# Optimization experiments

Hardware: AMD Instinct MI355X
Metric: run time of the kernel (lower is better)

## Reference

```python
import jax, jax.numpy as jnp
import numpy as np

N_NODES = 100000
N_EDGES = 1600000
IN_DIM, HID, OUT = 128, 128, 64


def setup_inputs() -> dict:
    key = jax.random.key(0)
    ks = jax.random.split(key, 8)
    x = jax.random.normal(ks[0], (N_NODES, IN_DIM), dtype=jnp.float32)
    edge_index = jax.random.randint(ks[1], (2, N_EDGES), 0, N_NODES, dtype=jnp.int64)
    # Glorot-ish init for GCNConv linear weights (stored as [in, out]).
    W1 = jax.random.normal(ks[2], (IN_DIM, HID), dtype=jnp.float32) * (1.0 / np.sqrt(IN_DIM))
    b1 = jnp.zeros((HID,), dtype=jnp.float32)
    W2 = jax.random.normal(ks[3], (HID, HID), dtype=jnp.float32) * (1.0 / np.sqrt(HID))
    b2 = jnp.zeros((HID,), dtype=jnp.float32)
    W3 = jax.random.normal(ks[4], (HID, OUT), dtype=jnp.float32) * (1.0 / np.sqrt(HID))
    b3 = jnp.zeros((OUT,), dtype=jnp.float32)
    return {"x": x, "W1": W1, "b1": b1, "W2": W2, "b2": b2,
            "W3": W3, "b3": b3, "edge_index": edge_index}


def _gcn_norm(edge_index, num_nodes):
    # GCNConv default: add self loops, symmetric normalization D^{-1/2} A D^{-1/2}.
    loops = jnp.arange(num_nodes, dtype=edge_index.dtype)
    src = jnp.concatenate([edge_index[0], loops])
    dst = jnp.concatenate([edge_index[1], loops])
    deg = jax.ops.segment_sum(jnp.ones_like(dst, dtype=jnp.float32), dst,
                              num_segments=num_nodes)
    dinv = jnp.where(deg > 0, jax.lax.rsqrt(deg), 0.0)
    norm = dinv[src] * dinv[dst]  # [E + N]
    return src, dst, norm


def _gcn_conv(h, W, b, src, dst, norm, num_nodes):
    h = h @ W                                   # transform first (PyG GCNConv)
    msg = h[src] * norm[:, None]                # gather + scale
    agg = jax.ops.segment_sum(msg, dst, num_segments=num_nodes)  # scatter-add
    return agg + b


def _dropout(h, key, p=0.5):
    keep = jax.random.bernoulli(key, 1.0 - p, h.shape)
    return jnp.where(keep, h / (1.0 - p), 0.0)


def reference(x, W1, b1, W2, b2, W3, b3, edge_index):
    num_nodes = x.shape[0]
    src, dst, norm = _gcn_norm(edge_index, num_nodes)
    kd1, kd2 = jax.random.split(jax.random.key(42))
    h = jax.nn.relu(_gcn_conv(x, W1, b1, src, dst, norm, num_nodes))
    h = _dropout(h, kd1)
    h = jax.nn.relu(_gcn_conv(h, W2, b2, src, dst, norm, num_nodes))
    h = _dropout(h, kd2)
    return _gcn_conv(h, W3, b3, src, dst, norm, num_nodes)
```

## Files before the change

kernel.cpp:

```cpp
#include <hip/hip_runtime.h>
#include <stdint.h>

#define NN 100000
#define NE 1600000
#define NMASKW 400000
#define GB_E 6250
#define GB_MASK 1563

typedef float f4 __attribute__((ext_vector_type(4)));
typedef float f2 __attribute__((ext_vector_type(2)));
typedef unsigned short us4 __attribute__((ext_vector_type(4)));
typedef short s16x8 __attribute__((ext_vector_type(8)));

__device__ inline float bf2f(unsigned short u) {
  return __uint_as_float(((uint32_t)u) << 16);
}
__device__ inline unsigned short f2bf(float f) {
  uint32_t u = __float_as_uint(f);
  return (unsigned short)((u + 0x7fffu + ((u >> 16) & 1u)) >> 16);
}
__device__ inline float lo16(uint32_t q) { return __uint_as_float(q << 16); }
__device__ inline float hi16(uint32_t q) { return __uint_as_float(q & 0xffff0000u); }

__host__ __device__ inline void threefry2x32(uint32_t k0, uint32_t k1,
                                             uint32_t x0, uint32_t x1,
                                             uint32_t* y0, uint32_t* y1) {
  uint32_t ks[3] = {k0, k1, k0 ^ k1 ^ 0x1BD11BDAu};
  x0 += ks[0]; x1 += ks[1];
  const uint32_t R[2][4] = {{13u, 15u, 26u, 6u}, {17u, 29u, 16u, 24u}};
#pragma unroll
  for (int i = 0; i < 5; ++i) {
#pragma unroll
    for (int j = 0; j < 4; ++j) {
      uint32_t r = R[i & 1][j];
      x0 += x1;
      x1 = (x1 << r) | (x1 >> (32u - r));
      x1 ^= x0;
    }
    x0 += ks[(i + 1) % 3];
    x1 += ks[(i + 2) % 3] + (uint32_t)(i + 1);
  }
  *y0 = x0; *y1 = x1;
}

__device__ inline uint32_t tf_bits32(uint32_t k0, uint32_t k1, uint32_t idx) {
  uint32_t a, b;
  threefry2x32(k0, k1, 0u, idx, &a, &b);
  return a ^ b;
}

__global__ __launch_bounds__(256) void k_histmask(
    const int* __restrict__ ei, uint32_t* __restrict__ cnt,
    int* __restrict__ slot, uint32_t* __restrict__ m1, uint32_t* __restrict__ m2,
    uint32_t k10, uint32_t k11, uint32_t k20, uint32_t k21) {
  int b = blockIdx.x;
  int q = b / 5, r = b % 5;
  if (r < 4) {
    int e = (q * 4 + r) * 256 + threadIdx.x;
    if (e < NE) {
      int d = ei[NE + e];
      slot[e] = (int)atomicAdd(&cnt[d], 1u);
    }
  } else {
    int t = q * 256 + threadIdx.x;
    if (t < NMASKW) {
      uint32_t base = (uint32_t)t * 32u;
      uint32_t w1 = 0, w2 = 0;
#pragma unroll 4
      for (int j = 0; j < 32; ++j) {
        w1 |= (tf_bits32(k10, k11, base + j) >> 31) << j;
        w2 |= (tf_bits32(k20, k21, base + j) >> 31) << j;
      }
      m1[t] = w1;
      m2[t] = w2;
    }
  }
}

__global__ __launch_bounds__(256) void k_scan1(const uint32_t* __restrict__ cnt,
                                               uint32_t* __restrict__ rp,
                                               uint32_t* __restrict__ bsum,
                                               float* __restrict__ dinv) {
  __shared__ uint32_t sh[256];
  int t = threadIdx.x;
  int base = blockIdx.x * 1024 + t * 4;
  uint32_t v[4];
  uint32_t s = 0;
#pragma unroll
  for (int i = 0; i < 4; ++i) {
    int idx = base + i;
    v[i] = (idx < NN) ? cnt[idx] : 0u;
    if (idx < NN) dinv[idx] = 1.0f / sqrtf((float)(v[i] + 1u));
    s += v[i];
  }
  sh[t] = s;
  __syncthreads();
  for (int off = 1; off < 256; off <<= 1) {
    uint32_t x = sh[t];
    if (t >= off) x += sh[t - off];
    __syncthreads();
    sh[t] = x;
    __syncthreads();
  }
  uint32_t run = (t > 0) ? sh[t - 1] : 0u;
  if (t == 255) bsum[blockIdx.x] = sh[255];
#pragma unroll
  for (int i = 0; i < 4; ++i) {
    int idx = base + i;
    if (idx < NN) rp[idx] = run;
    run += v[i];
  }
}

__global__ void k_scan2(uint32_t* bsum, int nb) {
  if (threadIdx.x == 0 && blockIdx.x == 0) {
    uint32_t s = 0;
    for (int i = 0; i < nb; ++i) { uint32_t x = bsum[i]; bsum[i] = s; s += x; }
  }
}

__global__ void k_scan3(uint32_t* rp, const uint32_t* __restrict__ bsum) {
  int i = blockIdx.x * 256 + threadIdx.x;
  if (i < NN) rp[i] += bsum[i >> 10];
  if (i == 0) rp[NN] = (uint32_t)NE;
}

__global__ void k_scatter(const int* __restrict__ ei,
                          const uint32_t* __restrict__ rp,
                          const int* __restrict__ slot,
                          const float* __restrict__ dinv,
                          uint2* __restrict__ e2) {
  int e = blockIdx.x * 256 + threadIdx.x;
  if (e < NE) {
    int s = ei[e];
    int d = ei[NE + e];
    float w = dinv[s] * dinv[d];
    uint32_t pos = rp[d] + (uint32_t)slot[e];
    uint2 rec;
    rec.x = (uint32_t)s;
    rec.y = __float_as_uint(w);
    e2[pos] = rec;
  }
}

__global__ void k_wsplit3(const float* __restrict__ W1, const float* __restrict__ W2,
                          const float* __restrict__ W3,
                          unsigned short* __restrict__ w1h, unsigned short* __restrict__ w1l,
                          unsigned short* __restrict__ w2h, unsigned short* __restrict__ w2l,
                          unsigned short* __restrict__ w3h, unsigned short* __restrict__ w3l) {
  int b = blockIdx.x;
  const float* W; unsigned short *H, *L; int dout, bb;
  if (b < 32)      { W = W1; H = w1h; L = w1l; dout = 128; bb = b; }
  else if (b < 64) { W = W2; H = w2h; L = w2l; dout = 128; bb = b - 32; }
  else             { W = W3; H = w3h; L = w3l; dout = 64;  bb = b - 64; }
  int lane = threadIdx.x;
  int kk = bb & 3;
  int ct = bb >> 2;
  int kbase = kk * 32 + (lane >> 4) * 8;
  int col = ct * 16 + (lane & 15);
  us4 h0, h1, l0, l1;
#pragma unroll
  for (int j = 0; j < 4; ++j) {
    float v = W[(size_t)(kbase + j) * dout + col];
    h0[j] = f2bf(v);
    l0[j] = f2bf(v - bf2f(h0[j]));
    float v2 = W[(size_t)(kbase + 4 + j) * dout + col];
    h1[j] = f2bf(v2);
    l1[j] = f2bf(v2 - bf2f(h1[j]));
  }
  size_t o = ((size_t)bb * 64 + lane) * 8;
  *(us4*)(H + o) = h0; *(us4*)(H + o + 4) = h1;
  *(us4*)(L + o) = l0; *(us4*)(L + o + 4) = l1;
}

__global__ __launch_bounds__(256) void k_gemm1(
    const float* __restrict__ A, const unsigned short* __restrict__ Wh,
    const unsigned short* __restrict__ Wl, unsigned short* __restrict__ C) {
  constexpr int NT = 8;
  const int w = threadIdx.x >> 6;
  const int lane = threadIdx.x & 63;
  const int row0 = blockIdx.x * 64 + w * 16;
  int ar = row0 + (lane & 15);
  if (ar >= NN) ar = NN - 1;
  const int aoff = (lane >> 4) * 8;
  s16x8 afh[4], afl[4];
#pragma unroll
  for (int kk = 0; kk < 4; ++kk) {
    f4 v0 = *(const f4*)(A + (size_t)ar * 128 + kk * 32 + aoff);
    f4 v1 = *(const f4*)(A + (size_t)ar * 128 + kk * 32 + aoff + 4);
#pragma unroll
    for (int j = 0; j < 4; ++j) {
      unsigned short h = f2bf(v0[j]);
      afh[kk][j] = (short)h;
      afl[kk][j] = (short)f2bf(v0[j] - bf2f(h));
      unsigned short h2 = f2bf(v1[j]);
      afh[kk][j + 4] = (short)h2;
      afl[kk][j + 4] = (short)f2bf(v1[j] - bf2f(h2));
    }
  }
  f4 acc[NT];
#pragma unroll
  for (int t = 0; t < NT; ++t) acc[t] = (f4){0.f, 0.f, 0.f, 0.f};
#pragma unroll
  for (int ct = 0; ct < NT; ++ct) {
#pragma unroll
    for (int kk = 0; kk < 4; ++kk) {
      size_t bo = ((size_t)(ct * 4 + kk) * 64 + lane) * 8;
      s16x8 bh = *(const s16x8*)(Wh + bo);
      s16x8 bl = *(const s16x8*)(Wl + bo);
      acc[ct] = __builtin_amdgcn_mfma_f32_16x16x32_bf16(afh[kk], bh, acc[ct], 0, 0, 0);
      acc[ct] = __builtin_amdgcn_mfma_f32_16x16x32_bf16(afh[kk], bl, acc[ct], 0, 0, 0);
      acc[ct] = __builtin_amdgcn_mfma_f32_16x16x32_bf16(afl[kk], bh, acc[ct], 0, 0, 0);
    }
  }
  const int rbase = row0 + (lane >> 4) * 4;
  const int cbase = lane & 15;
#pragma unroll
  for (int ct = 0; ct < NT; ++ct) {
#pragma unroll
    for (int r = 0; r < 4; ++r) {
      int gr = rbase + r;
      if (gr < NN) C[(size_t)gr * 128 + ct * 16 + cbase] = f2bf(acc[ct][r]);
    }
  }
}

template <int DOUT>
__global__ __launch_bounds__(256) void k_gemm_mfma(
    const unsigned short* __restrict__ Ah, const unsigned short* __restrict__ Al,
    const unsigned short* __restrict__ Wh, const unsigned short* __restrict__ Wl,
    unsigned short* __restrict__ C) {
  constexpr int NT = DOUT / 16;
  const int w = threadIdx.x >> 6;
  const int lane = threadIdx.x & 63;
  const int row0 = blockIdx.x * 64 + w * 16;
  int ar = row0 + (lane & 15);
  if (ar >= NN) ar = NN - 1;
  const int aoff = (lane >> 4) * 8;
  s16x8 afh[4], afl[4];
#pragma unroll
  for (int kk = 0; kk < 4; ++kk) {
    afh[kk] = *(const s16x8*)(Ah + (size_t)ar * 128 + kk * 32 + aoff);
    afl[kk] = *(const s16x8*)(Al + (size_t)ar * 128 + kk * 32 + aoff);
  }
  f4 acc[NT];
#pragma unroll
  for (int t = 0; t < NT; ++t) acc[t] = (f4){0.f, 0.f, 0.f, 0.f};
#pragma unroll
  for (int ct = 0; ct < NT; ++ct) {
#pragma unroll
    for (int kk = 0; kk < 4; ++kk) {
      size_t bo = ((size_t)(ct * 4 + kk) * 64 + lane) * 8;
      s16x8 bh = *(const s16x8*)(Wh + bo);
      s16x8 bl = *(const s16x8*)(Wl + bo);
      acc[ct] = __builtin_amdgcn_mfma_f32_16x16x32_bf16(afh[kk], bh, acc[ct], 0, 0, 0);
      acc[ct] = __builtin_amdgcn_mfma_f32_16x16x32_bf16(afh[kk], bl, acc[ct], 0, 0, 0);
      acc[ct] = __builtin_amdgcn_mfma_f32_16x16x32_bf16(afl[kk], bh, acc[ct], 0, 0, 0);
    }
  }
  const int rbase = row0 + (lane >> 4) * 4;
  const int cbase = lane & 15;
#pragma unroll
  for (int ct = 0; ct < NT; ++ct) {
#pragma unroll
    for (int r = 0; r < 4; ++r) {
      int gr = rbase + r;
      if (gr < NN) C[(size_t)gr * DOUT + ct * 16 + cbase] = f2bf(acc[ct][r]);
    }
  }
}

__global__ __launch_bounds__(256) void k_agg_mid(
    const unsigned short* __restrict__ hb, const uint32_t* __restrict__ rp,
    const uint2* __restrict__ e2, const float* __restrict__ dinv,
    const float* __restrict__ bias, const uint32_t* __restrict__ mask,
    unsigned short* __restrict__ oh, unsigned short* __restrict__ ol) {
  int wid = __builtin_amdgcn_readfirstlane(blockIdx.x * 4 + (threadIdx.x >> 6));
  if (wid >= NN) return;
  const int lane = threadIdx.x & 63;
  const int q = lane >> 4;
  const int fl = lane & 15;
  const uint32_t beg = rp[wid], end = rp[wid + 1];
  const float dv = dinv[wid];
  const float sn = dv * dv;
  const char* hbase = (const char*)hb;
  float acc[8];
#pragma unroll
  for (int j = 0; j < 8; ++j) acc[j] = 0.f;

  uint32_t u = beg;
  for (; u + 8 <= end; u += 8) {
    uint2 r0 = e2[u + q];
    uint2 r1 = e2[u + 4 + q];
    uint4 g0 = *(const uint4*)(hbase + ((size_t)r0.x << 8) + fl * 16);
    uint4 g1 = *(const uint4*)(hbase + ((size_t)r1.x << 8) + fl * 16);
    float w0 = __uint_as_float(r0.y), w1 = __uint_as_float(r1.y);
    acc[0] = fmaf(w0, lo16(g0.x), acc[0]); acc[1] = fmaf(w0, hi16(g0.x), acc[1]);
    acc[2] = fmaf(w0, lo16(g0.y), acc[2]); acc[3] = fmaf(w0, hi16(g0.y), acc[3]);
    acc[4] = fmaf(w0, lo16(g0.z), acc[4]); acc[5] = fmaf(w0, hi16(g0.z), acc[5]);
    acc[6] = fmaf(w0, lo16(g0.w), acc[6]); acc[7] = fmaf(w0, hi16(g0.w), acc[7]);
    acc[0] = fmaf(w1, lo16(g1.x), acc[0]); acc[1] = fmaf(w1, hi16(g1.x), acc[1]);
    acc[2] = fmaf(w1, lo16(g1.y), acc[2]); acc[3] = fmaf(w1, hi16(g1.y), acc[3]);
    acc[4] = fmaf(w1, lo16(g1.z), acc[4]); acc[5] = fmaf(w1, hi16(g1.z), acc[5]);
    acc[6] = fmaf(w1, lo16(g1.w), acc[6]); acc[7] = fmaf(w1, hi16(g1.w), acc[7]);
  }
  for (; u < end; u += 4) {
    uint32_t idx = u + (uint32_t)q;
    uint32_t cidx = idx < end ? idx : end - 1u;
    uint2 r = e2[cidx];
    float w = (idx < end) ? __uint_as_float(r.y) : 0.f;
    uint4 g = *(const uint4*)(hbase + ((size_t)r.x << 8) + fl * 16);
    acc[0] = fmaf(w, lo16(g.x), acc[0]); acc[1] = fmaf(w, hi16(g.x), acc[1]);
    acc[2] = fmaf(w, lo16(g.y), acc[2]); acc[3] = fmaf(w, hi16(g.y), acc[3]);
    acc[4] = fmaf(w, lo16(g.z), acc[4]); acc[5] = fmaf(w, hi16(g.z), acc[5]);
    acc[6] = fmaf(w, lo16(g.w), acc[6]); acc[7] = fmaf(w, hi16(g.w), acc[7]);
  }
#pragma unroll
  for (int j = 0; j < 8; ++j) acc[j] += __shfl_xor(acc[j], 16);
#pragma unroll
  for (int j = 0; j < 8; ++j) acc[j] += __shfl_xor(acc[j], 32);

  uint4 qs = *(const uint4*)(hbase + ((size_t)(uint32_t)wid << 8) + fl * 16);
  f4 b0 = *(const f4*)(bias + fl * 8);
  f4 b1 = *(const f4*)(bias + fl * 8 + 4);
  acc[0] = fmaf(sn, lo16(qs.x), acc[0]) + b0[0];
  acc[1] = fmaf(sn, hi16(qs.x), acc[1]) + b0[1];
  acc[2] = fmaf(sn, lo16(qs.y), acc[2]) + b0[2];
  acc[3] = fmaf(sn, hi16(qs.y), acc[3]) + b0[3];
  acc[4] = fmaf(sn, lo16(qs.z), acc[4]) + b1[0];
  acc[5] = fmaf(sn, hi16(qs.z), acc[5]) + b1[1];
  acc[6] = fmaf(sn, lo16(qs.w), acc[6]) + b1[2];
  acc[7] = fmaf(sn, hi16(qs.w), acc[7]) + b1[3];
  uint32_t mw = mask[(uint32_t)wid * 4u + (uint32_t)(fl >> 2)];
  uint32_t bb = (uint32_t)((fl & 3) * 8);
#pragma unroll
  for (int j = 0; j < 8; ++j) {
    float a = fmaxf(acc[j], 0.f);
    acc[j] = ((mw >> (bb + j)) & 1u) ? 0.f : a * 2.f;
  }
  uint32_t hw[4], lw[4];
#pragma unroll
  for (int j = 0; j < 4; ++j) {
    unsigned short h0 = f2bf(acc[2 * j]), h1 = f2bf(acc[2 * j + 1]);
    unsigned short g0 = f2bf(acc[2 * j] - bf2f(h0));
    unsigned short g1 = f2bf(acc[2 * j + 1] - bf2f(h1));
    hw[j] = (uint32_t)h0 | ((uint32_t)h1 << 16);
    lw[j] = (uint32_t)g0 | ((uint32_t)g1 << 16);
  }
  if (q == 0) {
    uint4 v = {hw[0], hw[1], hw[2], hw[3]};
    *(uint4*)(oh + (size_t)(uint32_t)wid * 128 + fl * 8) = v;
  } else if (q == 1) {
    uint4 v = {lw[0], lw[1], lw[2], lw[3]};
    *(uint4*)(ol + (size_t)(uint32_t)wid * 128 + fl * 8) = v;
  }
}

__global__ __launch_bounds__(256) void k_agg_final(
    const unsigned short* __restrict__ hb, const uint32_t* __restrict__ rp,
    const uint2* __restrict__ e2, const float* __restrict__ dinv,
    const float* __restrict__ bias, float* __restrict__ out) {
  int wid = __builtin_amdgcn_readfirstlane(blockIdx.x * 4 + (threadIdx.x >> 6));
  if (wid >= NN) return;
  const int lane = threadIdx.x & 63;
  const int q = lane >> 4;
  const int fl = lane & 15;
  const uint32_t beg = rp[wid], end = rp[wid + 1];
  const float dv = dinv[wid];
  const float sn = dv * dv;
  const char* hbase = (const char*)hb;
  float acc[4];
#pragma unroll
  for (int j = 0; j < 4; ++j) acc[j] = 0.f;

  uint32_t u = beg;
  for (; u + 8 <= end; u += 8) {
    uint2 r0 = e2[u + q];
    uint2 r1 = e2[u + 4 + q];
    uint2 g0 = *(const uint2*)(hbase + ((size_t)r0.x << 7) + fl * 8);
    uint2 g1 = *(const uint2*)(hbase + ((size_t)r1.x << 7) + fl * 8);
    float w0 = __uint_as_float(r0.y), w1 = __uint_as_float(r1.y);
    acc[0] = fmaf(w0, lo16(g0.x), acc[0]); acc[1] = fmaf(w0, hi16(g0.x), acc[1]);
    acc[2] = fmaf(w0, lo16(g0.y), acc[2]); acc[3] = fmaf(w0, hi16(g0.y), acc[3]);
    acc[0] = fmaf(w1, lo16(g1.x), acc[0]); acc[1] = fmaf(w1, hi16(g1.x), acc[1]);
    acc[2] = fmaf(w1, lo16(g1.y), acc[2]); acc[3] = fmaf(w1, hi16(g1.y), acc[3]);
  }
  for (; u < end; u += 4) {
    uint32_t idx = u + (uint32_t)q;
    uint32_t cidx = idx < end ? idx : end - 1u;
    uint2 r = e2[cidx];
    float w = (idx < end) ? __uint_as_float(r.y) : 0.f;
    uint2 g = *(const uint2*)(hbase + ((size_t)r.x << 7) + fl * 8);
    acc[0] = fmaf(w, lo16(g.x), acc[0]); acc[1] = fmaf(w, hi16(g.x), acc[1]);
    acc[2] = fmaf(w, lo16(g.y), acc[2]); acc[3] = fmaf(w, hi16(g.y), acc[3]);
  }
#pragma unroll
  for (int j = 0; j < 4; ++j) acc[j] += __shfl_xor(acc[j], 16);
#pragma unroll
  for (int j = 0; j < 4; ++j) acc[j] += __shfl_xor(acc[j], 32);

  uint2 qs = *(const uint2*)(hbase + ((size_t)(uint32_t)wid << 7) + fl * 8);
  f4 bv = *(const f4*)(bias + fl * 4);
  acc[0] = fmaf(sn, lo16(qs.x), acc[0]) + bv[0];
  acc[1] = fmaf(sn, hi16(qs.x), acc[1]) + bv[1];
  acc[2] = fmaf(sn, lo16(qs.y), acc[2]) + bv[2];
  acc[3] = fmaf(sn, hi16(qs.y), acc[3]) + bv[3];
  if (q == 0) {
    f4 v = {acc[0], acc[1], acc[2], acc[3]};
    *(f4*)(out + (size_t)(uint32_t)wid * 64 + fl * 4) = v;
  }
}

extern "C" void kernel_launch(void* const* d_in, const int* in_sizes, int n_in,
                              void* d_out, int out_size, void* d_ws, size_t ws_size,
                              hipStream_t stream) {
  (void)in_sizes; (void)n_in; (void)out_size; (void)ws_size;
  const float* x  = (const float*)d_in[0];
  const float* W1 = (const float*)d_in[1];
  const float* b1 = (const float*)d_in[2];
  const float* W2 = (const float*)d_in[3];
  const float* b2 = (const float*)d_in[4];
  const float* W3 = (const float*)d_in[5];
  const float* b3 = (const float*)d_in[6];
  const int* ei   = (const int*)d_in[7];
  float* out = (float*)d_out;

  char* p = (char*)d_ws;
  auto alloc = [&](size_t bytes) -> void* {
    void* r = (void*)p;
    p += (bytes + 255) & ~(size_t)255;
    return r;
  };
  uint32_t* cnt  = (uint32_t*)alloc((size_t)NN * 4);
  float*    dinv = (float*)alloc((size_t)NN * 4);
  uint32_t* rp   = (uint32_t*)alloc((size_t)(NN + 1) * 4);
  uint32_t* bsum = (uint32_t*)alloc(1024);
  int*      slot = (int*)alloc((size_t)NE * 4);
  uint2*    e2   = (uint2*)alloc((size_t)NE * 8);
  uint32_t* m1   = (uint32_t*)alloc((size_t)NMASKW * 4);
  uint32_t* m2   = (uint32_t*)alloc((size_t)NMASKW * 4);
  unsigned short* ah = (unsigned short*)alloc((size_t)NN * 128 * 2);
  unsigned short* al = (unsigned short*)alloc((size_t)NN * 128 * 2);
  unsigned short* hb = (unsigned short*)alloc((size_t)NN * 128 * 2);
  unsigned short* w1h = (unsigned short*)alloc(32 * 64 * 8 * 2);
  unsigned short* w1l = (unsigned short*)alloc(32 * 64 * 8 * 2);
  unsigned short* w2h = (unsigned short*)alloc(32 * 64 * 8 * 2);
  unsigned short* w2l = (unsigned short*)alloc(32 * 64 * 8 * 2);
  unsigned short* w3h = (unsigned short*)alloc(16 * 64 * 8 * 2);
  unsigned short* w3l = (unsigned short*)alloc(16 * 64 * 8 * 2);

  uint32_t kd1a, kd1b, kd2a, kd2b;
  threefry2x32(0u, 42u, 0u, 0u, &kd1a, &kd1b);
  threefry2x32(0u, 42u, 0u, 1u, &kd2a, &kd2b);

  const int gbN = (NN + 255) / 256;
  const int gbE = (NE + 255) / 256;
  const int gbScan = (NN + 1023) / 1024;
  const int gbGemm = (NN + 63) / 64;
  const int gbAgg = (NN + 3) / 4;

  hipMemsetAsync(cnt, 0, (size_t)NN * 4, stream);
  k_histmask<<<8000, 256, 0, stream>>>(ei, cnt, slot, m1, m2, kd1a, kd1b, kd2a, kd2b);
  k_scan1<<<gbScan, 256, 0, stream>>>(cnt, rp, bsum, dinv);
  k_scan2<<<1, 64, 0, stream>>>(bsum, gbScan);
  k_scan3<<<gbN, 256, 0, stream>>>(rp, bsum);
  k_scatter<<<gbE, 256, 0, stream>>>(ei, rp, slot, dinv, e2);
  k_wsplit3<<<80, 64, 0, stream>>>(W1, W2, W3, w1h, w1l, w2h, w2l, w3h, w3l);

  k_gemm1<<<gbGemm, 256, 0, stream>>>(x, w1h, w1l, hb);
  k_agg_mid<<<gbAgg, 256, 0, stream>>>(hb, rp, e2, dinv, b1, m1, ah, al);
  k_gemm_mfma<128><<<gbGemm, 256, 0, stream>>>(ah, al, w2h, w2l, hb);
  k_agg_mid<<<gbAgg, 256, 0, stream>>>(hb, rp, e2, dinv, b2, m2, ah, al);
  k_gemm_mfma<64><<<gbGemm, 256, 0, stream>>>(ah, al, w3h, w3l, hb);
  k_agg_final<<<gbAgg, 256, 0, stream>>>(hb, rp, e2, dinv, b3, out);
}
```

Before: 398.3 us.

## Store CSR as source indices only, compute edge weights on the fly in aggregation

The CSR edge array now holds only 4-byte source indices instead of 8-byte (src, weight) pairs, and the aggregation kernels recompute each edge weight as dinv[src]*dinv[dst] from a small cached table. The edge scatter and weight split are merged into one launch. The mask-generation blocks are reordered ahead of the histogram blocks. The aggregation loops are unrolled to 16 edges per iteration using packed float2 math. This halves edge-stream traffic in three aggregation passes and trims launches, at the cost of an extra dependent gather into dinv per edge.

```diff
diff --git a/kernel.cpp b/kernel.cpp
--- a/kernel.cpp
+++ b/kernel.cpp
@@ -4,8 +4,9 @@
 #define NN 100000
 #define NE 1600000
 #define NMASKW 400000
-#define GB_E 6250
-#define GB_MASK 1563
+#define MASK_BLKS 1563
+#define HIST_BLKS 6250
+#define WSPL_BLKS 20
 
 typedef float f4 __attribute__((ext_vector_type(4)));
 typedef float f2 __attribute__((ext_vector_type(2)));
@@ -54,15 +55,8 @@
     int* __restrict__ slot, uint32_t* __restrict__ m1, uint32_t* __restrict__ m2,
     uint32_t k10, uint32_t k11, uint32_t k20, uint32_t k21) {
   int b = blockIdx.x;
-  int q = b / 5, r = b % 5;
-  if (r < 4) {
-    int e = (q * 4 + r) * 256 + threadIdx.x;
-    if (e < NE) {
-      int d = ei[NE + e];
-      slot[e] = (int)atomicAdd(&cnt[d], 1u);
-    }
-  } else {
-    int t = q * 256 + threadIdx.x;
+  if (b < MASK_BLKS) {
+    int t = b * 256 + threadIdx.x;
     if (t < NMASKW) {
       uint32_t base = (uint32_t)t * 32u;
       uint32_t w1 = 0, w2 = 0;
@@ -74,6 +68,12 @@
       m1[t] = w1;
       m2[t] = w2;
     }
+  } else {
+    int e = (b - MASK_BLKS) * 256 + threadIdx.x;
+    if (e < NE) {
+      int d = ei[NE + e];
+      slot[e] = (int)atomicAdd(&cnt[d], 1u);
+    }
   }
 }
 
@@ -125,52 +125,47 @@
   if (i == 0) rp[NN] = (uint32_t)NE;
 }
 
-__global__ void k_scatter(const int* __restrict__ ei,
-                          const uint32_t* __restrict__ rp,
-                          const int* __restrict__ slot,
-                          const float* __restrict__ dinv,
-                          uint2* __restrict__ e2) {
-  int e = blockIdx.x * 256 + threadIdx.x;
-  if (e < NE) {
-    int s = ei[e];
-    int d = ei[NE + e];
-    float w = dinv[s] * dinv[d];
-    uint32_t pos = rp[d] + (uint32_t)slot[e];
-    uint2 rec;
-    rec.x = (uint32_t)s;
-    rec.y = __float_as_uint(w);
-    e2[pos] = rec;
-  }
-}
-
-__global__ void k_wsplit3(const float* __restrict__ W1, const float* __restrict__ W2,
-                          const float* __restrict__ W3,
-                          unsigned short* __restrict__ w1h, unsigned short* __restrict__ w1l,
-                          unsigned short* __restrict__ w2h, unsigned short* __restrict__ w2l,
-                          unsigned short* __restrict__ w3h, unsigned short* __restrict__ w3l) {
+__global__ __launch_bounds__(256) void k_scatwsplit(
+    const int* __restrict__ ei, const uint32_t* __restrict__ rp,
+    const int* __restrict__ slot, int* __restrict__ csrc,
+    const float* __restrict__ W1, const float* __restrict__ W2,
+    const float* __restrict__ W3,
+    unsigned short* __restrict__ w1h, unsigned short* __restrict__ w1l,
+    unsigned short* __restrict__ w2h, unsigned short* __restrict__ w2l,
+    unsigned short* __restrict__ w3h, unsigned short* __restrict__ w3l) {
   int b = blockIdx.x;
-  const float* W; unsigned short *H, *L; int dout, bb;
-  if (b < 32)      { W = W1; H = w1h; L = w1l; dout = 128; bb = b; }
-  else if (b < 64) { W = W2; H = w2h; L = w2l; dout = 128; bb = b - 32; }
-  else             { W = W3; H = w3h; L = w3l; dout = 64;  bb = b - 64; }
-  int lane = threadIdx.x;
-  int kk = bb & 3;
-  int ct = bb >> 2;
-  int kbase = kk * 32 + (lane >> 4) * 8;
-  int col = ct * 16 + (lane & 15);
-  us4 h0, h1, l0, l1;
-#pragma unroll
-  for (int j = 0; j < 4; ++j) {
-    float v = W[(size_t)(kbase + j) * dout + col];
-    h0[j] = f2bf(v);
-    l0[j] = f2bf(v - bf2f(h0[j]));
-    float v2 = W[(size_t)(kbase + 4 + j) * dout + col];
-    h1[j] = f2bf(v2);
-    l1[j] = f2bf(v2 - bf2f(h1[j]));
-  }
-  size_t o = ((size_t)bb * 64 + lane) * 8;
-  *(us4*)(H + o) = h0; *(us4*)(H + o + 4) = h1;
-  *(us4*)(L + o) = l0; *(us4*)(L + o + 4) = l1;
+  if (b < WSPL_BLKS) {
+    int bb = b * 4 + (threadIdx.x >> 6);
+    int lane = threadIdx.x & 63;
+    const float* W; unsigned short *H, *L; int dout, j0;
+    if (bb < 32)      { W = W1; H = w1h; L = w1l; dout = 128; j0 = bb; }
+    else if (bb < 64) { W = W2; H = w2h; L = w2l; dout = 128; j0 = bb - 32; }
+    else              { W = W3; H = w3h; L = w3l; dout = 64;  j0 = bb - 64; }
+    int kk = j0 & 3;
+    int ct = j0 >> 2;
+    int kbase = kk * 32 + (lane >> 4) * 8;
+    int col = ct * 16 + (lane & 15);
+    us4 h0, h1, l0, l1;
+#pragma unroll
+    for (int j = 0; j < 4; ++j) {
+      float v = W[(size_t)(kbase + j) * dout + col];
+      h0[j] = f2bf(v);
+      l0[j] = f2bf(v - bf2f(h0[j]));
+      float v2 = W[(size_t)(kbase + 4 + j) * dout + col];
+      h1[j] = f2bf(v2);
+      l1[j] = f2bf(v2 - bf2f(h1[j]));
+    }
+    size_t o = ((size_t)j0 * 64 + lane) * 8;
+    *(us4*)(H + o) = h0; *(us4*)(H + o + 4) = h1;
+    *(us4*)(L + o) = l0; *(us4*)(L + o + 4) = l1;
+  } else {
+    int e = (b - WSPL_BLKS) * 256 + threadIdx.x;
+    if (e < NE) {
+      int s = ei[e];
+      int d = ei[NE + e];
+      csrc[rp[d] + (uint32_t)slot[e]] = s;
+    }
+  }
 }
 
 __global__ __launch_bounds__(256) void k_gemm1(
@@ -272,7 +267,7 @@
 
 __global__ __launch_bounds__(256) void k_agg_mid(
     const unsigned short* __restrict__ hb, const uint32_t* __restrict__ rp,
-    const uint2* __restrict__ e2, const float* __restrict__ dinv,
+    const int* __restrict__ csrc, const float* __restrict__ dinv,
     const float* __restrict__ bias, const uint32_t* __restrict__ mask,
     unsigned short* __restrict__ oh, unsigned short* __restrict__ ol) {
   int wid = __builtin_amdgcn_readfirstlane(blockIdx.x * 4 + (threadIdx.x >> 6));
@@ -284,67 +279,74 @@
   const float dv = dinv[wid];
   const float sn = dv * dv;
   const char* hbase = (const char*)hb;
-  float acc[8];
-#pragma unroll
-  for (int j = 0; j < 8; ++j) acc[j] = 0.f;
+  f2 acc[4];
+#pragma unroll
+  for (int j = 0; j < 4; ++j) acc[j] = (f2){0.f, 0.f};
+
+#define ACC4(g, wv)                                                        \
+  {                                                                        \
+    f2 wv2 = {wv, wv};                                                     \
+    f2 h0 = {lo16(g.x), hi16(g.x)}; acc[0] += wv2 * h0;                    \
+    f2 h1 = {lo16(g.y), hi16(g.y)}; acc[1] += wv2 * h1;                    \
+    f2 h2 = {lo16(g.z), hi16(g.z)}; acc[2] += wv2 * h2;                    \
+    f2 h3 = {lo16(g.w), hi16(g.w)}; acc[3] += wv2 * h3;                    \
+  }
 
   uint32_t u = beg;
-  for (; u + 8 <= end; u += 8) {
-    uint2 r0 = e2[u + q];
-    uint2 r1 = e2[u + 4 + q];
-    uint4 g0 = *(const uint4*)(hbase + ((size_t)r0.x << 8) + fl * 16);
-    uint4 g1 = *(const uint4*)(hbase + ((size_t)r1.x << 8) + fl * 16);
-    float w0 = __uint_as_float(r0.y), w1 = __uint_as_float(r1.y);
-    acc[0] = fmaf(w0, lo16(g0.x), acc[0]); acc[1] = fmaf(w0, hi16(g0.x), acc[1]);
-    acc[2] = fmaf(w0, lo16(g0.y), acc[2]); acc[3] = fmaf(w0, hi16(g0.y), acc[3]);
-    acc[4] = fmaf(w0, lo16(g0.z), acc[4]); acc[5] = fmaf(w0, hi16(g0.z), acc[5]);
-    acc[6] = fmaf(w0, lo16(g0.w), acc[6]); acc[7] = fmaf(w0, hi16(g0.w), acc[7]);
-    acc[0] = fmaf(w1, lo16(g1.x), acc[0]); acc[1] = fmaf(w1, hi16(g1.x), acc[1]);
-    acc[2] = fmaf(w1, lo16(g1.y), acc[2]); acc[3] = fmaf(w1, hi16(g1.y), acc[3]);
-    acc[4] = fmaf(w1, lo16(g1.z), acc[4]); acc[5] = fmaf(w1, hi16(g1.z), acc[5]);
-    acc[6] = fmaf(w1, lo16(g1.w), acc[6]); acc[7] = fmaf(w1, hi16(g1.w), acc[7]);
+  for (; u + 16 <= end; u += 16) {
+    int s0 = csrc[u + q];
+    int s1 = csrc[u + 4 + q];
+    int s2 = csrc[u + 8 + q];
+    int s3 = csrc[u + 12 + q];
+    float w0 = dinv[s0] * dv, w1 = dinv[s1] * dv;
+    float w2 = dinv[s2] * dv, w3 = dinv[s3] * dv;
+    uint4 g0 = *(const uint4*)(hbase + ((size_t)(uint32_t)s0 << 8) + fl * 16);
+    uint4 g1 = *(const uint4*)(hbase + ((size_t)(uint32_t)s1 << 8) + fl * 16);
+    uint4 g2 = *(const uint4*)(hbase + ((size_t)(uint32_t)s2 << 8) + fl * 16);
+    uint4 g3 = *(const uint4*)(hbase + ((size_t)(uint32_t)s3 << 8) + fl * 16);
+    ACC4(g0, w0); ACC4(g1, w1); ACC4(g2, w2); ACC4(g3, w3);
   }
   for (; u < end; u += 4) {
     uint32_t idx = u + (uint32_t)q;
     uint32_t cidx = idx < end ? idx : end - 1u;
-    uint2 r = e2[cidx];
-    float w = (idx < end) ? __uint_as_float(r.y) : 0.f;
-    uint4 g = *(const uint4*)(hbase + ((size_t)r.x << 8) + fl * 16);
-    acc[0] = fmaf(w, lo16(g.x), acc[0]); acc[1] = fmaf(w, hi16(g.x), acc[1]);
-    acc[2] = fmaf(w, lo16(g.y), acc[2]); acc[3] = fmaf(w, hi16(g.y), acc[3]);
-    acc[4] = fmaf(w, lo16(g.z), acc[4]); acc[5] = fmaf(w, hi16(g.z), acc[5]);
-    acc[6] = fmaf(w, lo16(g.w), acc[6]); acc[7] = fmaf(w, hi16(g.w), acc[7]);
-  }
-#pragma unroll
-  for (int j = 0; j < 8; ++j) acc[j] += __shfl_xor(acc[j], 16);
-#pragma unroll
-  for (int j = 0; j < 8; ++j) acc[j] += __shfl_xor(acc[j], 32);
+    int s = csrc[cidx];
+    float w = (idx < end) ? dinv[s] * dv : 0.f;
+    uint4 g = *(const uint4*)(hbase + ((size_t)(uint32_t)s << 8) + fl * 16);
+    ACC4(g, w);
+  }
+#undef ACC4
+
+#pragma unroll
+  for (int j = 0; j < 4; ++j) {
+    acc[j][0] += __shfl_xor(acc[j][0], 16);
+    acc[j][1] += __shfl_xor(acc[j][1], 16);
+    acc[j][0] += __shfl_xor(acc[j][0], 32);
+    acc[j][1] += __shfl_xor(acc[j][1], 32);
+  }
 
   uint4 qs = *(const uint4*)(hbase + ((size_t)(uint32_t)wid << 8) + fl * 16);
-  f4 b0 = *(const f4*)(bias + fl * 8);
-  f4 b1 = *(const f4*)(bias + fl * 8 + 4);
-  acc[0] = fmaf(sn, lo16(qs.x), acc[0]) + b0[0];
-  acc[1] = fmaf(sn, hi16(qs.x), acc[1]) + b0[1];
-  acc[2] = fmaf(sn, lo16(qs.y), acc[2]) + b0[2];
-  acc[3] = fmaf(sn, hi16(qs.y), acc[3]) + b0[3];
-  acc[4] = fmaf(sn, lo16(qs.z), acc[4]) + b1[0];
-  acc[5] = fmaf(sn, hi16(qs.z), acc[5]) + b1[1];
-  acc[6] = fmaf(sn, lo16(qs.w), acc[6]) + b1[2];
-  acc[7] = fmaf(sn, hi16(qs.w), acc[7]) + b1[3];
+  f2 snv = {sn, sn};
+  f2 h0 = {lo16(qs.x), hi16(qs.x)};
+  f2 h1 = {lo16(qs.y), hi16(qs.y)};
+  f2 h2 = {lo16(qs.z), hi16(qs.z)};
+  f2 h3 = {lo16(qs.w), hi16(qs.w)};
+  acc[0] += snv * h0; acc[1] += snv * h1;
+  acc[2] += snv * h2; acc[3] += snv * h3;
+#pragma unroll
+  for (int j = 0; j < 4; ++j) acc[j] += *(const f2*)(bias + fl * 8 + 2 * j);
+
   uint32_t mw = mask[(uint32_t)wid * 4u + (uint32_t)(fl >> 2)];
   uint32_t bb = (uint32_t)((fl & 3) * 8);
-#pragma unroll
-  for (int j = 0; j < 8; ++j) {
-    float a = fmaxf(acc[j], 0.f);
-    acc[j] = ((mw >> (bb + j)) & 1u) ? 0.f : a * 2.f;
-  }
   uint32_t hw[4], lw[4];
 #pragma unroll
   for (int j = 0; j < 4; ++j) {
-    unsigned short h0 = f2bf(acc[2 * j]), h1 = f2bf(acc[2 * j + 1]);
-    unsigned short g0 = f2bf(acc[2 * j] - bf2f(h0));
-    unsigned short g1 = f2bf(acc[2 * j + 1] - bf2f(h1));
-    hw[j] = (uint32_t)h0 | ((uint32_t)h1 << 16);
+    float a0 = fmaxf(acc[j][0], 0.f);
+    float a1 = fmaxf(acc[j][1], 0.f);
+    a0 = ((mw >> (bb + 2 * j)) & 1u) ? 0.f : a0 * 2.f;
+    a1 = ((mw >> (bb + 2 * j + 1)) & 1u) ? 0.f : a1 * 2.f;
+    unsigned short hh0 = f2bf(a0), hh1 = f2bf(a1);
+    unsigned short g0 = f2bf(a0 - bf2f(hh0)), g1 = f2bf(a1 - bf2f(hh1));
+    hw[j] = (uint32_t)hh0 | ((uint32_t)hh1 << 16);
     lw[j] = (uint32_t)g0 | ((uint32_t)g1 << 16);
   }
   if (q == 0) {
@@ -358,7 +360,7 @@
 
 __global__ __launch_bounds__(256) void k_agg_final(
     const unsigned short* __restrict__ hb, const uint32_t* __restrict__ rp,
-    const uint2* __restrict__ e2, const float* __restrict__ dinv,
+    const int* __restrict__ csrc, const float* __restrict__ dinv,
     const float* __restrict__ bias, float* __restrict__ out) {
   int wid = __builtin_amdgcn_readfirstlane(blockIdx.x * 4 + (threadIdx.x >> 6));
   if (wid >= NN) return;
@@ -369,44 +371,59 @@
   const float dv = dinv[wid];
   const float sn = dv * dv;
   const char* hbase = (const char*)hb;
-  float acc[4];
-#pragma unroll
-  for (int j = 0; j < 4; ++j) acc[j] = 0.f;
+  f2 acc[2];
+  acc[0] = (f2){0.f, 0.f};
+  acc[1] = (f2){0.f, 0.f};
+
+#define ACC2(g, wv)                                                        \
+  {                                                                        \
+    f2 wv2 = {wv, wv};                                                     \
+    f2 h0 = {lo16(g.x), hi16(g.x)}; acc[0] += wv2 * h0;                    \
+    f2 h1 = {lo16(g.y), hi16(g.y)}; acc[1] += wv2 * h1;                    \
+  }
 
   uint32_t u = beg;
-  for (; u + 8 <= end; u += 8) {
-    uint2 r0 = e2[u + q];
-    uint2 r1 = e2[u + 4 + q];
-    uint2 g0 = *(const uint2*)(hbase + ((size_t)r0.x << 7) + fl * 8);
-    uint2 g1 = *(const uint2*)(hbase + ((size_t)r1.x << 7) + fl * 8);
-    float w0 = __uint_as_float(r0.y), w1 = __uint_as_float(r1.y);
-    acc[0] = fmaf(w0, lo16(g0.x), acc[0]); acc[1] = fmaf(w0, hi16(g0.x), acc[1]);
-    acc[2] = fmaf(w0, lo16(g0.y), acc[2]); acc[3] = fmaf(w0, hi16(g0.y), acc[3]);
-    acc[0] = fmaf(w1, lo16(g1.x), acc[0]); acc[1] = fmaf(w1, hi16(g1.x), acc[1]);
-    acc[2] = fmaf(w1, lo16(g1.y), acc[2]); acc[3] = fmaf(w1, hi16(g1.y), acc[3]);
+  for (; u + 16 <= end; u += 16) {
+    int s0 = csrc[u + q];
+    int s1 = csrc[u + 4 + q];
+    int s2 = csrc[u + 8 + q];
+    int s3 = csrc[u + 12 + q];
+    float w0 = dinv[s0] * dv, w1 = dinv[s1] * dv;
+    float w2 = dinv[s2] * dv, w3 = dinv[s3] * dv;
+    uint2 g0 = *(const uint2*)(hbase + ((size_t)(uint32_t)s0 << 7) + fl * 8);
+    uint2 g1 = *(const uint2*)(hbase + ((size_t)(uint32_t)s1 << 7) + fl * 8);
+    uint2 g2 = *(const uint2*)(hbase + ((size_t)(uint32_t)s2 << 7) + fl * 8);
+    uint2 g3 = *(const uint2*)(hbase + ((size_t)(uint32_t)s3 << 7) + fl * 8);
+    ACC2(g0, w0); ACC2(g1, w1); ACC2(g2, w2); ACC2(g3, w3);
   }
   for (; u < end; u += 4) {
     uint32_t idx = u + (uint32_t)q;
     uint32_t cidx = idx < end ? idx : end - 1u;
-    uint2 r = e2[cidx];
-    float w = (idx < end) ? __uint_as_float(r.y) : 0.f;
-    uint2 g = *(const uint2*)(hbase + ((size_t)r.x << 7) + fl * 8);
-    acc[0] = fmaf(w, lo16(g.x), acc[0]); acc[1] = fmaf(w, hi16(g.x), acc[1]);
-    acc[2] = fmaf(w, lo16(g.y), acc[2]); acc[3] = fmaf(w, hi16(g.y), acc[3]);
-  }
-#pragma unroll
-  for (int j = 0; j < 4; ++j) acc[j] += __shfl_xor(acc[j], 16);
-#pragma unroll
-  for (int j = 0; j < 4; ++j) acc[j] += __shfl_xor(acc[j], 32);
+    int s = csrc[cidx];
+    float w = (idx < end) ? dinv[s] * dv : 0.f;
+    uint2 g = *(const uint2*)(hbase + ((size_t)(uint32_t)s << 7) + fl * 8);
+    ACC2(g, w);
+  }
+#undef ACC2
+
+#pragma unroll
+  for (int j = 0; j < 2; ++j) {
+    acc[j][0] += __shfl_xor(acc[j][0], 16);
+    acc[j][1] += __shfl_xor(acc[j][1], 16);
+    acc[j][0] += __shfl_xor(acc[j][0], 32);
+    acc[j][1] += __shfl_xor(acc[j][1], 32);
+  }
 
   uint2 qs = *(const uint2*)(hbase + ((size_t)(uint32_t)wid << 7) + fl * 8);
-  f4 bv = *(const f4*)(bias + fl * 4);
-  acc[0] = fmaf(sn, lo16(qs.x), acc[0]) + bv[0];
-  acc[1] = fmaf(sn, hi16(qs.x), acc[1]) + bv[1];
-  acc[2] = fmaf(sn, lo16(qs.y), acc[2]) + bv[2];
-  acc[3] = fmaf(sn, hi16(qs.y), acc[3]) + bv[3];
+  f2 snv = {sn, sn};
+  f2 h0 = {lo16(qs.x), hi16(qs.x)};
+  f2 h1 = {lo16(qs.y), hi16(qs.y)};
+  acc[0] += snv * h0;
+  acc[1] += snv * h1;
+  acc[0] += *(const f2*)(bias + fl * 4);
+  acc[1] += *(const f2*)(bias + fl * 4 + 2);
   if (q == 0) {
-    f4 v = {acc[0], acc[1], acc[2], acc[3]};
+    f4 v = {acc[0][0], acc[0][1], acc[1][0], acc[1][1]};
     *(f4*)(out + (size_t)(uint32_t)wid * 64 + fl * 4) = v;
   }
 }
@@ -436,7 +453,7 @@
   uint32_t* rp   = (uint32_t*)alloc((size_t)(NN + 1) * 4);
   uint32_t* bsum = (uint32_t*)alloc(1024);
   int*      slot = (int*)alloc((size_t)NE * 4);
-  uint2*    e2   = (uint2*)alloc((size_t)NE * 8);
+  int*      csrc = (int*)alloc((size_t)NE * 4);
   uint32_t* m1   = (uint32_t*)alloc((size_t)NMASKW * 4);
   uint32_t* m2   = (uint32_t*)alloc((size_t)NMASKW * 4);
   unsigned short* ah = (unsigned short*)alloc((size_t)NN * 128 * 2);
@@ -454,23 +471,23 @@
   threefry2x32(0u, 42u, 0u, 1u, &kd2a, &kd2b);
 
   const int gbN = (NN + 255) / 256;
-  const int gbE = (NE + 255) / 256;
   const int gbScan = (NN + 1023) / 1024;
   const int gbGemm = (NN + 63) / 64;
   const int gbAgg = (NN + 3) / 4;
 
   hipMemsetAsync(cnt, 0, (size_t)NN * 4, stream);
-  k_histmask<<<8000, 256, 0, stream>>>(ei, cnt, slot, m1, m2, kd1a, kd1b, kd2a, kd2b);
+  k_histmask<<<MASK_BLKS + HIST_BLKS, 256, 0, stream>>>(
+      ei, cnt, slot, m1, m2, kd1a, kd1b, kd2a, kd2b);
   k_scan1<<<gbScan, 256, 0, stream>>>(cnt, rp, bsum, dinv);
   k_scan2<<<1, 64, 0, stream>>>(bsum, gbScan);
   k_scan3<<<gbN, 256, 0, stream>>>(rp, bsum);
-  k_scatter<<<gbE, 256, 0, stream>>>(ei, rp, slot, dinv, e2);
-  k_wsplit3<<<80, 64, 0, stream>>>(W1, W2, W3, w1h, w1l, w2h, w2l, w3h, w3l);
+  k_scatwsplit<<<WSPL_BLKS + HIST_BLKS, 256, 0, stream>>>(
+      ei, rp, slot, csrc, W1, W2, W3, w1h, w1l, w2h, w2l, w3h, w3l);
 
   k_gemm1<<<gbGemm, 256, 0, stream>>>(x, w1h, w1l, hb);
-  k_agg_mid<<<gbAgg, 256, 0, stream>>>(hb, rp, e2, dinv, b1, m1, ah, al);
+  k_agg_mid<<<gbAgg, 256, 0, stream>>>(hb, rp, csrc, dinv, b1, m1, ah, al);
   k_gemm_mfma<128><<<gbGemm, 256, 0, stream>>>(ah, al, w2h, w2l, hb);
-  k_agg_mid<<<gbAgg, 256, 0, stream>>>(hb, rp, e2, dinv, b2, m2, ah, al);
+  k_agg_mid<<<gbAgg, 256, 0, stream>>>(hb, rp, csrc, dinv, b2, m2, ah, al);
   k_gemm_mfma<64><<<gbGemm, 256, 0, stream>>>(ah, al, w3h, w3l, hb);
-  k_agg_final<<<gbAgg, 256, 0, stream>>>(hb, rp, e2, dinv, b3, out);
-}
+  k_agg_final<<<gbAgg, 256, 0, stream>>>(hb, rp, csrc, dinv, b3, out);
+}
```

Result: slower. 426.5 us (+7.1%).
